# Optimization experiments

Measured on AMD Instinct MI355X. Metric: run time of the kernel, lower is better.

## Reference

```python
import jax, jax.numpy as jnp
import numpy as np

H, D, IN, E, N = 4, 16, 64, 400000, 100000
RELS = [("c1c1", "C1", "C1"), ("c1c2", "C1", "C2"), ("c1c3", "C1", "C3"),
        ("c2c1", "C2", "C1"), ("c2c2", "C2", "C2"), ("c2c3", "C2", "C3"),
        ("c3c1", "C3", "C1"), ("c3c2", "C3", "C2"), ("c3c3", "C3", "C3")]
TYPES = ("C1", "C2", "C3")


def setup_inputs() -> dict:
    key = jax.random.key(0)
    ks = iter(jax.random.split(key, 128))
    inp = {}
    for t in TYPES:
        inp["feat_" + t] = jax.random.normal(next(ks), (N, IN), jnp.float32)
        inp["W_" + t] = jax.random.normal(next(ks), (IN, H * D), jnp.float32) * 0.05
        inp["b_" + t] = jnp.zeros((H * D,), jnp.float32)
    for r, s, d in RELS:
        inp["W_" + r] = jax.random.normal(next(ks), (IN, H * D), jnp.float32) * 0.05
        inp["b_" + r] = jnp.zeros((H * D,), jnp.float32)
        inp["asrc_" + r] = jax.random.normal(next(ks), (H, D), jnp.float32) * 0.1
        inp["adst_" + r] = jax.random.normal(next(ks), (H, D), jnp.float32) * 0.1
        inp["src_" + r] = jax.random.randint(next(ks), (E,), 0, N, jnp.int32)
        inp["dst_" + r] = jax.random.randint(next(ks), (E,), 0, N, jnp.int32)
    return inp


def _forward(feats, selfp, relp):
    # leaky_relu with negative_slope = l_alpha = 0.2
    lrelu = lambda x: jnp.where(x >= 0, x, 0.2 * x)
    # per-type self projections Wh_T  [N, H, D]
    Wh_self = {t: (feats[t] @ selfp[t][0] + selfp[t][1]).reshape(-1, H, D) for t in TYPES}
    agg = {t: jnp.zeros((feats[t].shape[0], H, D), feats[t].dtype) for t in TYPES}
    for r, s, d in RELS:
        W, b, asrc, adst, src, dst = relp[r]
        # project once per source node, then gather per edge (same math as per-edge fc)
        Wh = (feats[s] @ W + b).reshape(-1, H, D)      # [Ns, H, D]
        whe = Wh[src]                                   # [E, H, D]
        # attention logits: (Wh_e * a_src).sum(-1) + (Wh_self_dst * a_dst).sum(-1)
        e = lrelu((whe * asrc).sum(-1) + (Wh_self[d][dst] * adst).sum(-1))  # [E, H]
        # nn.Softmax(dim=1) in the original acts over the heads axis of [E, H, 1]
        alpha = jax.nn.softmax(e, axis=1)[..., None]    # [E, H, 1]
        agg[d] = agg[d] + jax.ops.segment_sum(whe * alpha, dst, num_segments=agg[d].shape[0])
    return tuple(jax.nn.relu(agg[t]) for t in TYPES)


def reference(feat_C1, feat_C2, feat_C3, W_C1, b_C1, W_C2, b_C2, W_C3, b_C3,
              W_c1c1, b_c1c1, asrc_c1c1, adst_c1c1, src_c1c1, dst_c1c1,
              W_c1c2, b_c1c2, asrc_c1c2, adst_c1c2, src_c1c2, dst_c1c2,
              W_c1c3, b_c1c3, asrc_c1c3, adst_c1c3, src_c1c3, dst_c1c3,
              W_c2c1, b_c2c1, asrc_c2c1, adst_c2c1, src_c2c1, dst_c2c1,
              W_c2c2, b_c2c2, asrc_c2c2, adst_c2c2, src_c2c2, dst_c2c2,
              W_c2c3, b_c2c3, asrc_c2c3, adst_c2c3, src_c2c3, dst_c2c3,
              W_c3c1, b_c3c1, asrc_c3c1, adst_c3c1, src_c3c1, dst_c3c1,
              W_c3c2, b_c3c2, asrc_c3c2, adst_c3c2, src_c3c2, dst_c3c2,
              W_c3c3, b_c3c3, asrc_c3c3, adst_c3c3, src_c3c3, dst_c3c3):
    L = dict(locals())
    feats = {t: L["feat_" + t] for t in TYPES}
    selfp = {t: (L["W_" + t], L["b_" + t]) for t in TYPES}
    relp = {r: (L["W_" + r], L["b_" + r], L["asrc_" + r], L["adst_" + r], L["src_" + r], L["dst_" + r]) for r, _, _ in RELS}
    return _forward(feats, selfp, relp)
```

## Files before the change

### kernel.cpp

```cpp
#include <hip/hip_runtime.h>
#include <hip/hip_bf16.h>

constexpr int IN_F = 64;
constexpr int HD   = 64;

constexpr int BW_BITS = 10;
constexpr int BWIDTH  = 1 << BW_BITS;
constexpr int BCAP    = 6144;
constexpr int BIN_EPT = 16;
constexpr int BIN_CHUNK = 256 * BIN_EPT;

constexpr int PROJ_ROWS  = 128;
constexpr int LDS_STRIDE = 72;
constexpr int NJOBS      = 18;

typedef __attribute__((ext_vector_type(8))) short short8;
typedef __attribute__((ext_vector_type(4))) float floatx4;
typedef __attribute__((ext_vector_type(4))) unsigned short us4;

static __device__ __forceinline__ float bf2f(unsigned short u) {
  union { unsigned int i; float f; } c; c.i = ((unsigned int)u) << 16; return c.f;
}
static __device__ __forceinline__ unsigned short f2bf_bits(float f) {
  union { __hip_bfloat16 h; unsigned short u; } c; c.h = __float2bfloat16(f); return c.u;
}

struct PrepParams {
  const float* W[3][4];
  const float* b[3][4];
  const float* asrc[9];
  const float* adst[9];
  unsigned short* Bpack;
  float* biasPack;
};

__global__ __launch_bounds__(64) void prep_kernel(PrepParams pp) {
  const int t = blockIdx.x / NJOBS;
  const int j = blockIdx.x % NJOBS;
  const int lane = threadIdx.x;
  const int q = lane >> 4, n = lane & 15;

  const float* W; const float* bv; const float* av = nullptr;
  int n0 = 0; bool dotjob;
  if (j < 3) {
    W = pp.W[t][0]; bv = pp.b[t][0]; av = pp.adst[j * 3 + t]; dotjob = true;
  } else {
    const int jj = j - 3, p = jj / 5, sub = jj % 5;
    W = pp.W[t][1 + p]; bv = pp.b[t][1 + p];
    if (sub < 4) { n0 = sub * 16; dotjob = false; }
    else { av = pp.asrc[t * 3 + p]; dotjob = true; }
  }

  unsigned short* outB = pp.Bpack + (size_t)(t * NJOBS + j) * 2 * 64 * 8;
  for (int kt = 0; kt < 2; ++kt) {
    for (int jj = 0; jj < 8; ++jj) {
      const int k = kt * 32 + q * 8 + jj;
      float v = 0.f;
      if (!dotjob) v = W[k * 64 + n0 + n];
      else if (n < 4) {
        for (int d = 0; d < 16; ++d) v += W[k * 64 + n * 16 + d] * av[n * 16 + d];
      }
      outB[(kt * 64 + lane) * 8 + jj] = f2bf_bits(v);
    }
  }
  if (lane < 16) {
    float v = 0.f;
    if (!dotjob) v = bv[n0 + lane];
    else if (lane < 4) {
      for (int d = 0; d < 16; ++d) v += bv[lane * 16 + d] * av[lane * 16 + d];
    }
    pp.biasPack[(t * NJOBS + j) * 16 + lane] = v;
  }
}

struct ProjParams {
  const float* feat[3];
  const unsigned short* Bpack;
  const float* biasPack;
  unsigned short* wh[9];
  float* sdot[9];
  float* ddot[9];
  int N;
};

__global__ __launch_bounds__(256) void proj_kernel(ProjParams p) {
  const int t = blockIdx.y;
  const int n0blk = blockIdx.x * PROJ_ROWS;
  const int tid = threadIdx.x;
  const int N = p.N;

  __shared__ unsigned short featL[PROJ_ROWS * LDS_STRIDE];

  {
    const float* feat = p.feat[t];
    #pragma unroll
    for (int c = 0; c < 8; ++c) {
      const int flat = c * 256 + tid;
      const int row = flat >> 4;
      const int c4  = (flat & 15) << 2;
      const int gr = n0blk + row;
      float4 v = make_float4(0.f, 0.f, 0.f, 0.f);
      if (gr < N) v = *(const float4*)(feat + (size_t)gr * IN_F + c4);
      ushort4 o;
      o.x = f2bf_bits(v.x); o.y = f2bf_bits(v.y);
      o.z = f2bf_bits(v.z); o.w = f2bf_bits(v.w);
      *(ushort4*)(featL + row * LDS_STRIDE + c4) = o;
    }
  }
  __syncthreads();

  const int wave = tid >> 6;
  const int lane = tid & 63;
  const int q = lane >> 4, l15 = lane & 15;

  short8 afrag[2][2];
  #pragma unroll
  for (int mt = 0; mt < 2; ++mt) {
    const int row = wave * 32 + mt * 16 + l15;
    #pragma unroll
    for (int kt = 0; kt < 2; ++kt) {
      afrag[mt][kt] = *(const short8*)(featL + row * LDS_STRIDE + kt * 32 + q * 8);
    }
  }

  const unsigned short* Bbase = p.Bpack + (size_t)t * NJOBS * 2 * 64 * 8;
  const float* biasBase = p.biasPack + (size_t)t * NJOBS * 16;

  short8 b0 = *(const short8*)(Bbase + 0 * 512 + lane * 8);
  short8 b1 = *(const short8*)(Bbase + 1 * 512 + lane * 8);
  float bias = biasBase[l15];

  for (int j = 0; j < NJOBS; ++j) {
    short8 b0n, b1n; float biasn = 0.f;
    if (j + 1 < NJOBS) {
      b0n = *(const short8*)(Bbase + ((size_t)(j + 1) * 2 + 0) * 512 + lane * 8);
      b1n = *(const short8*)(Bbase + ((size_t)(j + 1) * 2 + 1) * 512 + lane * 8);
      biasn = biasBase[(j + 1) * 16 + l15];
    }

    #pragma unroll
    for (int mt = 0; mt < 2; ++mt) {
      floatx4 acc = {bias, bias, bias, bias};
      acc = __builtin_amdgcn_mfma_f32_16x16x32_bf16(afrag[mt][0], b0, acc, 0, 0, 0);
      acc = __builtin_amdgcn_mfma_f32_16x16x32_bf16(afrag[mt][1], b1, acc, 0, 0, 0);
      const int rbase = n0blk + wave * 32 + mt * 16 + q * 4;
      if (j < 3) {
        if (l15 < 4) {
          float* dp = p.ddot[j * 3 + t];
          #pragma unroll
          for (int r = 0; r < 4; ++r) {
            const int gr = rbase + r;
            if (gr < N) dp[(size_t)gr * 4 + l15] = acc[r];
          }
        }
      } else {
        const int jj = j - 3, pidx = jj / 5, sub = jj % 5, ri = t * 3 + pidx;
        if (sub < 4) {
          unsigned short* whp = p.wh[ri];
          #pragma unroll
          for (int r = 0; r < 4; ++r) {
            const int gr = rbase + r;
            if (gr < N) whp[(size_t)gr * HD + sub * 16 + l15] = f2bf_bits(acc[r]);
          }
        } else if (l15 < 4) {
          float* sp = p.sdot[ri];
          #pragma unroll
          for (int r = 0; r < 4; ++r) {
            const int gr = rbase + r;
            if (gr < N) sp[(size_t)gr * 4 + l15] = acc[r];
          }
        }
      }
    }
    b0 = b0n; b1 = b1n; bias = biasn;
  }
}

struct EdgeLists { const int* src[9]; const int* dst[9]; int E; int N; };

__global__ __launch_bounds__(256) void zero_u32_kernel(unsigned* p, int n) {
  const int i = blockIdx.x * 256 + threadIdx.x;
  if (i < n) p[i] = 0u;
}

__global__ __launch_bounds__(256) void bin_kernel(EdgeLists el, unsigned* bcnt,
                                                  unsigned* binBuf, int nbuck) {
  const int r   = blockIdx.y;
  const int tid = threadIdx.x;
  const int e0  = blockIdx.x * BIN_CHUNK;
  const int E   = el.E;
  const int* srcp = el.src[r];
  const int* dstp = el.dst[r];

  __shared__ unsigned bh[128], bcur[128], bbase[128];
  if (tid < 128) { bh[tid] = 0u; bcur[tid] = 0u; }
  __syncthreads();

  int sv[BIN_EPT], dv[BIN_EPT];
  #pragma unroll
  for (int i = 0; i < BIN_EPT; ++i) {
    const int e = e0 + i * 256 + tid;
    if (e < E) {
      sv[i] = srcp[e];
      dv[i] = dstp[e];
      atomicAdd(&bh[dv[i] >> BW_BITS], 1u);
    } else dv[i] = -1;
  }
  __syncthreads();

  if (tid < 128) {
    bbase[tid] = (tid < nbuck && bh[tid] > 0u)
                   ? atomicAdd(bcnt + (size_t)r * nbuck + tid, bh[tid]) : 0u;
  }
  __syncthreads();

  unsigned* bb = binBuf + (size_t)r * nbuck * BCAP;
  #pragma unroll
  for (int i = 0; i < BIN_EPT; ++i) {
    if (dv[i] >= 0) {
      const int b = dv[i] >> BW_BITS;
      const unsigned pos = bbase[b] + atomicAdd(&bcur[b], 1u);
      if (pos < (unsigned)BCAP)
        bb[(size_t)b * BCAP + pos] = (unsigned)sv[i] | ((unsigned)(dv[i] & (BWIDTH - 1)) << 17);
    }
  }
}

struct CsrParams {
  const unsigned* binBuf;
  const unsigned* bcnt;
  unsigned* offsets;
  unsigned* perm;
  unsigned short* alf;
  const float* sdot[9];
  const float* ddot[9];
  int N, E, nbuck;
};

__global__ __launch_bounds__(256) void csr_kernel(CsrParams cp) {
  const int r   = blockIdx.y;
  const int b   = blockIdx.x;
  const int tid = threadIdx.x;
  const int N = cp.N, E = cp.E, nbuck = cp.nbuck;
  const unsigned* bcr = cp.bcnt + (size_t)r * nbuck;
  unsigned* offr = cp.offsets + (size_t)r * (N + 1);
  unsigned* permr = cp.perm + (size_t)r * E;
  unsigned short* alfr = cp.alf + (size_t)r * E * 4;
  const float* sdr = cp.sdot[r];
  const float* ddr = cp.ddot[r];

  __shared__ unsigned S[BWIDTH];
  __shared__ unsigned T[256];
  __shared__ unsigned permL[BCAP];

  unsigned pre = (tid < b) ? bcr[tid] : 0u;
  if (pre > (unsigned)BCAP) pre = BCAP;
  pre += __shfl_xor(pre, 1);  pre += __shfl_xor(pre, 2);
  pre += __shfl_xor(pre, 4);  pre += __shfl_xor(pre, 8);
  pre += __shfl_xor(pre, 16); pre += __shfl_xor(pre, 32);
  if ((tid & 63) == 0) T[tid >> 6] = pre;
  unsigned cnt = bcr[b];
  if (cnt > (unsigned)BCAP) cnt = BCAP;
  __syncthreads();
  const unsigned base = T[0] + T[1] + T[2] + T[3];
  __syncthreads();

  const unsigned* buf = cp.binBuf + ((size_t)r * nbuck + b) * BCAP;

  for (int i = tid; i < BWIDTH; i += 256) S[i] = 0u;
  __syncthreads();

  for (unsigned i = tid; i < cnt; i += 256) atomicAdd(&S[buf[i] >> 17], 1u);
  __syncthreads();

  const int b4 = tid * 4;
  unsigned loc0 = S[b4], loc1 = S[b4 + 1], loc2 = S[b4 + 2], loc3 = S[b4 + 3];
  unsigned s = loc0 + loc1 + loc2 + loc3;
  T[tid] = s;
  __syncthreads();
  for (int d = 1; d < 256; d <<= 1) {
    const unsigned v = T[tid];
    const unsigned a = (tid >= d) ? T[tid - d] : 0u;
    __syncthreads();
    T[tid] = v + a;
    __syncthreads();
  }
  unsigned run = T[tid] - s;
  S[b4]     = run;  run += loc0;
  S[b4 + 1] = run;  run += loc1;
  S[b4 + 2] = run;  run += loc2;
  S[b4 + 3] = run;
  __syncthreads();

  const int d0 = b * BWIDTH;
  for (int i = tid; i < BWIDTH; i += 256) {
    const int d = d0 + i;
    if (d < N) offr[d] = base + S[i];
  }
  if (b == 0 && tid == 0) offr[N] = (unsigned)E;
  __syncthreads();

  for (unsigned i = tid; i < cnt; i += 256) {
    const unsigned v = buf[i];
    const unsigned pos = atomicAdd(&S[v >> 17], 1u);
    permL[pos] = v;
  }
  __syncthreads();

  for (unsigned i = tid; i < cnt; i += 256) {
    const unsigned v = permL[i];
    const unsigned sv = v & 0x1FFFFu;
    const int dn = d0 + (int)(v >> 17);
    permr[base + i] = sv;

    const float4 sd = *(const float4*)(sdr + (size_t)sv * 4);
    const float4 dd = *(const float4*)(ddr + (size_t)dn * 4);
    float e0 = sd.x + dd.x, e1 = sd.y + dd.y, e2 = sd.z + dd.z, e3 = sd.w + dd.w;
    e0 = (e0 >= 0.f) ? e0 : 0.2f * e0;
    e1 = (e1 >= 0.f) ? e1 : 0.2f * e1;
    e2 = (e2 >= 0.f) ? e2 : 0.2f * e2;
    e3 = (e3 >= 0.f) ? e3 : 0.2f * e3;
    const float m = fmaxf(fmaxf(e0, e1), fmaxf(e2, e3));
    const float x0 = __expf(e0 - m);
    const float x1 = __expf(e1 - m);
    const float x2 = __expf(e2 - m);
    const float x3 = __expf(e3 - m);
    const float inv = 1.f / (x0 + x1 + x2 + x3);
    uint2 packed;
    packed.x = ((unsigned)f2bf_bits(x1 * inv) << 16) | f2bf_bits(x0 * inv);
    packed.y = ((unsigned)f2bf_bits(x3 * inv) << 16) | f2bf_bits(x2 * inv);
    *(uint2*)(alfr + (size_t)(base + i) * 4) = packed;
  }
}

struct AggParams {
  const unsigned* offsets[9];
  const unsigned* perm[9];
  const unsigned short* alf[9];
  const unsigned short* wh[9];
  float* outp[3];
  int N, E;
};

__global__ __launch_bounds__(256) void agg_kernel(AggParams p) {
  const int t    = blockIdx.y;
  const int w    = threadIdx.x >> 6;
  const int lane = threadIdx.x & 63;
  const int n    = blockIdx.x * 4 + w;
  if (n >= p.N) return;
  const int slot = lane >> 4;
  const int l16  = lane & 15;
  const int h    = l16 >> 2;

  unsigned st[3], en[3];
  const unsigned* __restrict__ pm[3];
  const unsigned short* __restrict__ al[3];
  const unsigned short* __restrict__ whr[3];
  #pragma unroll
  for (int sj = 0; sj < 3; ++sj) {
    const int r = sj * 3 + t;
    pm[sj]  = p.perm[r];
    al[sj]  = p.alf[r];
    whr[sj] = p.wh[r];
    st[sj]  = p.offsets[r][n];
    en[sj]  = p.offsets[r][n + 1];
  }

  float acc0 = 0.f, acc1 = 0.f, acc2 = 0.f, acc3 = 0.f;

  unsigned svA[3], svB[3];
  float aA[3], aB[3];
  #pragma unroll
  for (int sj = 0; sj < 3; ++sj) {
    const unsigned s = st[sj], e = en[sj];
    const unsigned posA = s + slot;
    const unsigned pcA  = (e > s)     ? ((posA < e) ? posA : e - 1) : 0u;
    const unsigned posB = s + 4 + slot;
    const unsigned pcB  = (e > s + 4) ? ((posB < e) ? posB : e - 1) : 0u;
    svA[sj] = pm[sj][pcA];
    svB[sj] = pm[sj][pcB];
    aA[sj] = (posA < e) ? bf2f(al[sj][pcA * 4 + h]) : 0.f;
    aB[sj] = (posB < e) ? bf2f(al[sj][pcB * 4 + h]) : 0.f;
  }

  us4 wvA[3], wvB[3];
  #pragma unroll
  for (int sj = 0; sj < 3; ++sj) {
    wvA[sj] = *(const us4*)(whr[sj] + (size_t)svA[sj] * HD + l16 * 4);
    wvB[sj] = *(const us4*)(whr[sj] + (size_t)svB[sj] * HD + l16 * 4);
  }

  #pragma unroll
  for (int sj = 0; sj < 3; ++sj) {
    acc0 = fmaf(aA[sj], bf2f(wvA[sj].x), acc0);
    acc1 = fmaf(aA[sj], bf2f(wvA[sj].y), acc1);
    acc2 = fmaf(aA[sj], bf2f(wvA[sj].z), acc2);
    acc3 = fmaf(aA[sj], bf2f(wvA[sj].w), acc3);
    acc0 = fmaf(aB[sj], bf2f(wvB[sj].x), acc0);
    acc1 = fmaf(aB[sj], bf2f(wvB[sj].y), acc1);
    acc2 = fmaf(aB[sj], bf2f(wvB[sj].z), acc2);
    acc3 = fmaf(aB[sj], bf2f(wvB[sj].w), acc3);
  }

  #pragma unroll
  for (int sj = 0; sj < 3; ++sj) {
    const unsigned e = en[sj];
    for (unsigned bse = st[sj] + 8; bse < e; bse += 4) {
      const unsigned pos  = bse + slot;
      const unsigned posc = (pos < e) ? pos : e - 1;
      const unsigned s = pm[sj][posc];
      float a = bf2f(al[sj][posc * 4 + h]);
      if (pos >= e) a = 0.f;
      const us4 wv = *(const us4*)(whr[sj] + (size_t)s * HD + l16 * 4);
      acc0 = fmaf(a, bf2f(wv.x), acc0);
      acc1 = fmaf(a, bf2f(wv.y), acc1);
      acc2 = fmaf(a, bf2f(wv.z), acc2);
      acc3 = fmaf(a, bf2f(wv.w), acc3);
    }
  }

  acc0 += __shfl_xor(acc0, 16); acc1 += __shfl_xor(acc1, 16);
  acc2 += __shfl_xor(acc2, 16); acc3 += __shfl_xor(acc3, 16);
  acc0 += __shfl_xor(acc0, 32); acc1 += __shfl_xor(acc1, 32);
  acc2 += __shfl_xor(acc2, 32); acc3 += __shfl_xor(acc3, 32);

  if (slot == 0) {
    float4 v;
    v.x = fmaxf(acc0, 0.f); v.y = fmaxf(acc1, 0.f);
    v.z = fmaxf(acc2, 0.f); v.w = fmaxf(acc3, 0.f);
    *(float4*)(p.outp[t] + (size_t)n * HD + l16 * 4) = v;
  }
}

extern "C" void kernel_launch(void* const* d_in, const int* in_sizes, int n_in,
                              void* d_out, int out_size, void* d_ws, size_t ws_size,
                              hipStream_t stream) {
  const int N = in_sizes[0] / IN_F;
  const int E = in_sizes[9 + 4];
  const int nbuck = (N + BWIDTH - 1) >> BW_BITS;

  ProjParams pp; AggParams ap; EdgeLists el; CsrParams cp; PrepParams qq;
  pp.N = N; ap.N = N; ap.E = E; el.E = E; el.N = N;
  cp.N = N; cp.E = E; cp.nbuck = nbuck;

  for (int t = 0; t < 3; ++t) {
    pp.feat[t] = (const float*)d_in[t * 3 + 0];
    qq.W[t][0] = (const float*)d_in[t * 3 + 1];
    qq.b[t][0] = (const float*)d_in[t * 3 + 2];
    for (int j = 0; j < 3; ++j) {
      const int base = 9 + (t * 3 + j) * 6;
      qq.W[t][1 + j] = (const float*)d_in[base + 0];
      qq.b[t][1 + j] = (const float*)d_in[base + 1];
    }
  }

  char* ws = (char*)d_ws;
  const size_t whBytes  = (size_t)N * HD * sizeof(__hip_bfloat16);
  const size_t dotBytes = (size_t)N * 4 * sizeof(float);
  char* whBase   = ws;
  char* sdotBase = whBase + 9 * whBytes;
  char* ddotBase = sdotBase + 9 * dotBytes;
  unsigned* offsets = (unsigned*)(ddotBase + 9 * dotBytes);
  unsigned* bcnt    = offsets + (size_t)9 * (N + 1);
  unsigned* perm    = bcnt + (size_t)9 * ((nbuck + 63) & ~63);
  unsigned short* alf = (unsigned short*)(perm + (size_t)9 * E);
  unsigned* binBuf  = (unsigned*)(alf + (size_t)9 * E * 4);
  unsigned short* Bpack = (unsigned short*)(binBuf + (size_t)9 * nbuck * BCAP);
  float* biasPack = (float*)(Bpack + (size_t)3 * NJOBS * 2 * 64 * 8);

  cp.offsets = offsets; cp.perm = perm; cp.alf = alf;
  cp.binBuf = binBuf; cp.bcnt = bcnt;
  qq.Bpack = Bpack; qq.biasPack = biasPack;
  pp.Bpack = Bpack; pp.biasPack = biasPack;

  for (int ri = 0; ri < 9; ++ri) {
    const int base = 9 + ri * 6;
    qq.asrc[ri] = (const float*)d_in[base + 2];
    qq.adst[ri] = (const float*)d_in[base + 3];
    pp.wh[ri]   = (unsigned short*)(whBase + (size_t)ri * whBytes);
    pp.sdot[ri] = (float*)(sdotBase + (size_t)ri * dotBytes);
    pp.ddot[ri] = (float*)(ddotBase + (size_t)ri * dotBytes);
    el.src[ri]  = (const int*)d_in[base + 4];
    el.dst[ri]  = (const int*)d_in[base + 5];
    cp.sdot[ri] = pp.sdot[ri];
    cp.ddot[ri] = pp.ddot[ri];
    ap.wh[ri]   = pp.wh[ri];
    ap.alf[ri]  = alf + (size_t)ri * E * 4;
    ap.offsets[ri] = offsets + (size_t)ri * (N + 1);
    ap.perm[ri]    = perm + (size_t)ri * E;
  }
  for (int t = 0; t < 3; ++t) ap.outp[t] = (float*)d_out + (size_t)t * N * HD;

  prep_kernel<<<dim3(3 * NJOBS), 64, 0, stream>>>(qq);

  const int nbc = 9 * nbuck;
  zero_u32_kernel<<<dim3((nbc + 255) / 256), 256, 0, stream>>>(bcnt, nbc);
  bin_kernel<<<dim3((E + BIN_CHUNK - 1) / BIN_CHUNK, 9), 256, 0, stream>>>(el, bcnt, binBuf, nbuck);

  proj_kernel<<<dim3((N + PROJ_ROWS - 1) / PROJ_ROWS, 3), 256, 0, stream>>>(pp);

  csr_kernel<<<dim3(nbuck, 9), 256, 0, stream>>>(cp);

  agg_kernel<<<dim3((N + 3) / 4, 3), 256, 0, stream>>>(ap);
}
```

Baseline: 555.4 us.

## Stage projection outputs in LDS for coalesced stores; widen agg gathers to 16B

The projection kernel now writes each relation's bf16 Wh tile into the reused LDS feature buffer and then stores full rows to global memory as 16-byte vectors, replacing scattered 2-byte stores. The aggregation kernel switches to 8 lanes per edge, each loading 8 bf16 values, so each wave processes 8 edges per iteration instead of 4, with one extra shuffle stage in the reduction. The goal is fewer, wider memory transactions on both the write and gather paths. The cost is an extra barrier and LDS round-trip in the projection kernel, and more live registers in aggregation. The first 8-edge prologue now covers only 8 edges, where before it issued two 4-edge batches.

After: 541.7 us. 2.5% less time.

```diff
diff --git a/kernel.cpp b/kernel.cpp
--- a/kernel.cpp
+++ b/kernel.cpp
@@ -17,6 +17,7 @@
 typedef __attribute__((ext_vector_type(8))) short short8;
 typedef __attribute__((ext_vector_type(4))) float floatx4;
 typedef __attribute__((ext_vector_type(4))) unsigned short us4;
+typedef __attribute__((ext_vector_type(8))) unsigned short us8;
 
 static __device__ __forceinline__ float bf2f(unsigned short u) {
   union { unsigned int i; float f; } c; c.i = ((unsigned int)u) << 16; return c.f;
@@ -122,6 +123,7 @@
       afrag[mt][kt] = *(const short8*)(featL + row * LDS_STRIDE + kt * 32 + q * 8);
     }
   }
+  __syncthreads();
 
   const unsigned short* Bbase = p.Bpack + (size_t)t * NJOBS * 2 * 64 * 8;
   const float* biasBase = p.biasPack + (size_t)t * NJOBS * 16;
@@ -143,35 +145,49 @@
       floatx4 acc = {bias, bias, bias, bias};
       acc = __builtin_amdgcn_mfma_f32_16x16x32_bf16(afrag[mt][0], b0, acc, 0, 0, 0);
       acc = __builtin_amdgcn_mfma_f32_16x16x32_bf16(afrag[mt][1], b1, acc, 0, 0, 0);
-      const int rbase = n0blk + wave * 32 + mt * 16 + q * 4;
+      const int lrbase = wave * 32 + mt * 16 + q * 4;
       if (j < 3) {
         if (l15 < 4) {
           float* dp = p.ddot[j * 3 + t];
           #pragma unroll
           for (int r = 0; r < 4; ++r) {
-            const int gr = rbase + r;
+            const int gr = n0blk + lrbase + r;
             if (gr < N) dp[(size_t)gr * 4 + l15] = acc[r];
           }
         }
       } else {
         const int jj = j - 3, pidx = jj / 5, sub = jj % 5, ri = t * 3 + pidx;
         if (sub < 4) {
-          unsigned short* whp = p.wh[ri];
           #pragma unroll
           for (int r = 0; r < 4; ++r) {
-            const int gr = rbase + r;
-            if (gr < N) whp[(size_t)gr * HD + sub * 16 + l15] = f2bf_bits(acc[r]);
+            featL[(lrbase + r) * LDS_STRIDE + sub * 16 + l15] = f2bf_bits(acc[r]);
           }
         } else if (l15 < 4) {
           float* sp = p.sdot[ri];
           #pragma unroll
           for (int r = 0; r < 4; ++r) {
-            const int gr = rbase + r;
+            const int gr = n0blk + lrbase + r;
             if (gr < N) sp[(size_t)gr * 4 + l15] = acc[r];
           }
         }
       }
     }
+
+    if (j >= 3 && ((j - 3) % 5) == 3) {
+      const int ri = t * 3 + (j - 3) / 5;
+      unsigned short* whp = p.wh[ri];
+      const int lr = wave * 32 + (lane >> 1);
+      const int gr = n0blk + lr;
+      const int c0 = (lane & 1) * 32;
+      if (gr < N) {
+        #pragma unroll
+        for (int k2 = 0; k2 < 4; ++k2) {
+          us8 v = *(const us8*)(featL + lr * LDS_STRIDE + c0 + k2 * 8);
+          *(us8*)(whp + (size_t)gr * HD + c0 + k2 * 8) = v;
+        }
+      }
+    }
+
     b0 = b0n; b1 = b1n; bias = biasn;
   }
 }
@@ -348,9 +364,9 @@
   const int lane = threadIdx.x & 63;
   const int n    = blockIdx.x * 4 + w;
   if (n >= p.N) return;
-  const int slot = lane >> 4;
-  const int l16  = lane & 15;
-  const int h    = l16 >> 2;
+  const int slot = lane >> 3;
+  const int l8   = lane & 7;
+  const int h    = l8 >> 1;
 
   unsigned st[3], en[3];
   const unsigned* __restrict__ pm[3];
@@ -366,69 +382,66 @@
     en[sj]  = p.offsets[r][n + 1];
   }
 
-  float acc0 = 0.f, acc1 = 0.f, acc2 = 0.f, acc3 = 0.f;
-
-  unsigned svA[3], svB[3];
-  float aA[3], aB[3];
+  float acc[8];
+  #pragma unroll
+  for (int k = 0; k < 8; ++k) acc[k] = 0.f;
+
+  unsigned sv[3]; float a[3];
   #pragma unroll
   for (int sj = 0; sj < 3; ++sj) {
     const unsigned s = st[sj], e = en[sj];
-    const unsigned posA = s + slot;
-    const unsigned pcA  = (e > s)     ? ((posA < e) ? posA : e - 1) : 0u;
-    const unsigned posB = s + 4 + slot;
-    const unsigned pcB  = (e > s + 4) ? ((posB < e) ? posB : e - 1) : 0u;
-    svA[sj] = pm[sj][pcA];
-    svB[sj] = pm[sj][pcB];
-    aA[sj] = (posA < e) ? bf2f(al[sj][pcA * 4 + h]) : 0.f;
-    aB[sj] = (posB < e) ? bf2f(al[sj][pcB * 4 + h]) : 0.f;
-  }
-
-  us4 wvA[3], wvB[3];
+    const unsigned pos = s + slot;
+    const unsigned pc  = (e > s) ? ((pos < e) ? pos : e - 1) : 0u;
+    sv[sj] = pm[sj][pc];
+    a[sj]  = (pos < e) ? bf2f(al[sj][pc * 4 + h]) : 0.f;
+  }
+
+  us8 wv[3];
   #pragma unroll
   for (int sj = 0; sj < 3; ++sj) {
-    wvA[sj] = *(const us4*)(whr[sj] + (size_t)svA[sj] * HD + l16 * 4);
-    wvB[sj] = *(const us4*)(whr[sj] + (size_t)svB[sj] * HD + l16 * 4);
+    wv[sj] = *(const us8*)(whr[sj] + (size_t)sv[sj] * HD + l8 * 8);
   }
 
   #pragma unroll
   for (int sj = 0; sj < 3; ++sj) {
-    acc0 = fmaf(aA[sj], bf2f(wvA[sj].x), acc0);
-    acc1 = fmaf(aA[sj], bf2f(wvA[sj].y), acc1);
-    acc2 = fmaf(aA[sj], bf2f(wvA[sj].z), acc2);
-    acc3 = fmaf(aA[sj], bf2f(wvA[sj].w), acc3);
-    acc0 = fmaf(aB[sj], bf2f(wvB[sj].x), acc0);
-    acc1 = fmaf(aB[sj], bf2f(wvB[sj].y), acc1);
-    acc2 = fmaf(aB[sj], bf2f(wvB[sj].z), acc2);
-    acc3 = fmaf(aB[sj], bf2f(wvB[sj].w), acc3);
+    #pragma unroll
+    for (int k = 0; k < 8; ++k) {
+      acc[k] = fmaf(a[sj], bf2f(wv[sj][k]), acc[k]);
+    }
   }
 
   #pragma unroll
   for (int sj = 0; sj < 3; ++sj) {
     const unsigned e = en[sj];
-    for (unsigned bse = st[sj] + 8; bse < e; bse += 4) {
+    for (unsigned bse = st[sj] + 8; bse < e; bse += 8) {
       const unsigned pos  = bse + slot;
       const unsigned posc = (pos < e) ? pos : e - 1;
-      const unsigned s = pm[sj][posc];
-      float a = bf2f(al[sj][posc * 4 + h]);
-      if (pos >= e) a = 0.f;
-      const us4 wv = *(const us4*)(whr[sj] + (size_t)s * HD + l16 * 4);
-      acc0 = fmaf(a, bf2f(wv.x), acc0);
-      acc1 = fmaf(a, bf2f(wv.y), acc1);
-      acc2 = fmaf(a, bf2f(wv.z), acc2);
-      acc3 = fmaf(a, bf2f(wv.w), acc3);
-    }
-  }
-
-  acc0 += __shfl_xor(acc0, 16); acc1 += __shfl_xor(acc1, 16);
-  acc2 += __shfl_xor(acc2, 16); acc3 += __shfl_xor(acc3, 16);
-  acc0 += __shfl_xor(acc0, 32); acc1 += __shfl_xor(acc1, 32);
-  acc2 += __shfl_xor(acc2, 32); acc3 += __shfl_xor(acc3, 32);
+      const unsigned s2 = pm[sj][posc];
+      const float a2 = (pos < e) ? bf2f(al[sj][posc * 4 + h]) : 0.f;
+      const us8 wv2 = *(const us8*)(whr[sj] + (size_t)s2 * HD + l8 * 8);
+      #pragma unroll
+      for (int k = 0; k < 8; ++k) {
+        acc[k] = fmaf(a2, bf2f(wv2[k]), acc[k]);
+      }
+    }
+  }
+
+  #pragma unroll
+  for (int k = 0; k < 8; ++k) {
+    acc[k] += __shfl_xor(acc[k], 8);
+    acc[k] += __shfl_xor(acc[k], 16);
+    acc[k] += __shfl_xor(acc[k], 32);
+  }
 
   if (slot == 0) {
-    float4 v;
-    v.x = fmaxf(acc0, 0.f); v.y = fmaxf(acc1, 0.f);
-    v.z = fmaxf(acc2, 0.f); v.w = fmaxf(acc3, 0.f);
-    *(float4*)(p.outp[t] + (size_t)n * HD + l16 * 4) = v;
+    float4 v0, v1;
+    v0.x = fmaxf(acc[0], 0.f); v0.y = fmaxf(acc[1], 0.f);
+    v0.z = fmaxf(acc[2], 0.f); v0.w = fmaxf(acc[3], 0.f);
+    v1.x = fmaxf(acc[4], 0.f); v1.y = fmaxf(acc[5], 0.f);
+    v1.z = fmaxf(acc[6], 0.f); v1.w = fmaxf(acc[7], 0.f);
+    float* op = p.outp[t] + (size_t)n * HD + l8 * 8;
+    *(float4*)(op) = v0;
+    *(float4*)(op + 4) = v1;
   }
 }
 
```
